# Kernel tuning notes

Hardware: AMD Instinct MI355X
Metric: run time of the kernel (lower is better)

The kernel has to match this reference:

```python
import jax, jax.numpy as jnp
import numpy as np

N, K, D = 32768, 32, 128


def setup_inputs() -> dict:
    key = jax.random.key(0)
    ks = jax.random.split(key, 8)
    return {
        "x1": jax.random.normal(ks[0], (N, D), dtype=jnp.float32),
        "dists_argmax_1": jax.random.randint(ks[1], (N, K), 0, N),
        "dists_max_1": jax.random.uniform(ks[2], (N, K), dtype=jnp.float32),
        "x2": jax.random.normal(ks[3], (N, D), dtype=jnp.float32),
        "dists_argmax_2": jax.random.randint(ks[4], (N, K), 0, N),
        "dists_max_2": jax.random.uniform(ks[5], (N, K), dtype=jnp.float32),
        "w_out": jax.random.normal(ks[6], (1, D), dtype=jnp.float32) * (1.0 / np.sqrt(D)),
        "b_out": jnp.zeros((1,), dtype=jnp.float32),
    }


def _branch(x, idx, dmax, w_out, b_out):
    # anchor gather: [N,K,D]
    anchor = x[idx]
    # mcf 'default': distance-scaled anchor features (self_features unused)
    msgs = dmax[..., None] * anchor  # [N,K,D]
    # linear_out_position then squeeze(-1): [N,K]
    out_pos = jnp.einsum("nkd,d->nk", msgs, w_out[0]) + b_out[0]
    # agg 'mean' over anchor dim: [N,D]
    out_struct = jnp.mean(msgs, axis=1)
    return out_pos, out_struct


def reference(x1, dists_argmax_1, dists_max_1, x2, dists_argmax_2, dists_max_2, w_out, b_out):
    op1, os1 = _branch(x1, dists_argmax_1, dists_max_1, w_out, b_out)
    op2, os2 = _branch(x2, dists_argmax_2, dists_max_2, w_out, b_out)
    return (op1, os1, op2, os2)
```

## Files before the change

### kernel.cpp

```cpp
#include <hip/hip_runtime.h>

#define NN 32768
#define KK 32
#define DD 128

typedef float v2f __attribute__((ext_vector_type(2)));
typedef float v4f __attribute__((ext_vector_type(4)));
typedef int   v4i __attribute__((ext_vector_type(4)));

__global__ __launch_bounds__(256) void prep_kernel(const float* __restrict__ x1,
                                                   const float* __restrict__ x2,
                                                   const float* __restrict__ w,
                                                   unsigned int* __restrict__ x8,
                                                   float* __restrict__ xw) {
    const int wave = threadIdx.x >> 6;
    const int lane = threadIdx.x & 63;
    const int half = lane >> 5;
    const int c    = lane & 31;
    const int row  = blockIdx.x * 8 + wave * 2 + half;
    const float* x = (row < NN) ? (x1 + (size_t)row * DD)
                                : (x2 + (size_t)(row - NN) * DD);
    const v4f xv = __builtin_nontemporal_load((const v4f*)(x + 4 * c));
    const float4 wv = *(const float4*)(w + 4 * c);

    int packed = __builtin_amdgcn_cvt_pk_fp8_f32(xv.x, xv.y, 0, false);
    packed     = __builtin_amdgcn_cvt_pk_fp8_f32(xv.z, xv.w, packed, true);
    x8[(size_t)row * 32 + c] = (unsigned int)packed;

    float s = xv.x * wv.x + xv.y * wv.y + xv.z * wv.z + xv.w * wv.w;
    #pragma unroll
    for (int m = 16; m >= 1; m >>= 1)
        s += __shfl_xor(s, m, 64);
    if (c == 0) xw[row] = s;
}

__global__ __launch_bounds__(256) void pgnn_main(
    const uint4* __restrict__ x8,
    const float* __restrict__ xw,
    const int* __restrict__ idx1, const float* __restrict__ dm1,
    const int* __restrict__ idx2, const float* __restrict__ dm2,
    const float* __restrict__ b_out,
    float* __restrict__ out)
{
    const int g      = blockIdx.x;
    const int xcd    = g & 7;
    const int branch = xcd >> 2;
    const int nb     = (g >> 3) * 4 + (xcd & 3);

    const uint4* __restrict__ xb  = x8 + (size_t)branch * NN * 8;
    const float* __restrict__ xwb = xw + (size_t)branch * NN;
    const int*   __restrict__ idx = branch ? idx2 : idx1;
    const float* __restrict__ dm  = branch ? dm2  : dm1;
    float* __restrict__ op = out + (size_t)branch * ((size_t)NN * KK + (size_t)NN * DD);
    float* __restrict__ os = op + (size_t)NN * KK;

    __shared__ uint2 s_pair[32][KK + 2];

    const int tid = threadIdx.x;
    const int n0  = nb * 32;

    {
        const int rr = tid >> 3;
        const int k4 = (tid & 7) * 4;
        const size_t off = (size_t)(n0 + rr) * KK + k4;
        const v4i iv = __builtin_nontemporal_load((const v4i*)(idx + off));
        const v4f dv = __builtin_nontemporal_load((const v4f*)(dm + off));
        const float bb = b_out[0];
        v4f o = { dv.x * xwb[iv.x] + bb, dv.y * xwb[iv.y] + bb,
                  dv.z * xwb[iv.z] + bb, dv.w * xwb[iv.w] + bb };
        __builtin_nontemporal_store(o, (v4f*)(op + off));
        s_pair[rr][k4 + 0] = make_uint2((unsigned)iv.x, __float_as_uint(dv.x));
        s_pair[rr][k4 + 1] = make_uint2((unsigned)iv.y, __float_as_uint(dv.y));
        s_pair[rr][k4 + 2] = make_uint2((unsigned)iv.z, __float_as_uint(dv.z));
        s_pair[rr][k4 + 3] = make_uint2((unsigned)iv.w, __float_as_uint(dv.w));
    }
    __syncthreads();

    const int sub = tid >> 3;
    const int h   = tid & 7;
    const uint2* __restrict__ prow = s_pair[sub];

    float a[16];
    #pragma unroll
    for (int i = 0; i < 16; ++i) a[i] = 0.f;

    #pragma unroll
    for (int kb = 0; kb < KK; kb += 4) {
        const uint4 pq0 = *(const uint4*)&prow[kb];
        const uint4 pq1 = *(const uint4*)&prow[kb + 2];
        uint4 u[4];
        u[0] = xb[pq0.x * 8u + h];
        u[1] = xb[pq0.z * 8u + h];
        u[2] = xb[pq1.x * 8u + h];
        u[3] = xb[pq1.z * 8u + h];
        const float dd4[4] = { __uint_as_float(pq0.y), __uint_as_float(pq0.w),
                               __uint_as_float(pq1.y), __uint_as_float(pq1.w) };
        #pragma unroll
        for (int j = 0; j < 4; ++j) {
            const float d = dd4[j];
            const v2f f0 = __builtin_amdgcn_cvt_pk_f32_fp8((int)u[j].x, false);
            const v2f f1 = __builtin_amdgcn_cvt_pk_f32_fp8((int)u[j].x, true);
            const v2f f2 = __builtin_amdgcn_cvt_pk_f32_fp8((int)u[j].y, false);
            const v2f f3 = __builtin_amdgcn_cvt_pk_f32_fp8((int)u[j].y, true);
            const v2f f4 = __builtin_amdgcn_cvt_pk_f32_fp8((int)u[j].z, false);
            const v2f f5 = __builtin_amdgcn_cvt_pk_f32_fp8((int)u[j].z, true);
            const v2f f6 = __builtin_amdgcn_cvt_pk_f32_fp8((int)u[j].w, false);
            const v2f f7 = __builtin_amdgcn_cvt_pk_f32_fp8((int)u[j].w, true);
            a[0]  += d * f0.x; a[1]  += d * f0.y; a[2]  += d * f1.x; a[3]  += d * f1.y;
            a[4]  += d * f2.x; a[5]  += d * f2.y; a[6]  += d * f3.x; a[7]  += d * f3.y;
            a[8]  += d * f4.x; a[9]  += d * f4.y; a[10] += d * f5.x; a[11] += d * f5.y;
            a[12] += d * f6.x; a[13] += d * f6.y; a[14] += d * f7.x; a[15] += d * f7.y;
        }
    }
    const float inv = 1.0f / KK;
    float* dst = os + (size_t)(n0 + sub) * DD + h * 16;
    v4f o0 = { a[0]  * inv, a[1]  * inv, a[2]  * inv, a[3]  * inv };
    v4f o1 = { a[4]  * inv, a[5]  * inv, a[6]  * inv, a[7]  * inv };
    v4f o2 = { a[8]  * inv, a[9]  * inv, a[10] * inv, a[11] * inv };
    v4f o3 = { a[12] * inv, a[13] * inv, a[14] * inv, a[15] * inv };
    __builtin_nontemporal_store(o0, (v4f*)dst);
    __builtin_nontemporal_store(o1, (v4f*)(dst + 4));
    __builtin_nontemporal_store(o2, (v4f*)(dst + 8));
    __builtin_nontemporal_store(o3, (v4f*)(dst + 12));
}

__global__ __launch_bounds__(256) void pgnn_fused(
    const float* __restrict__ x1, const int* __restrict__ idx1,
    const float* __restrict__ dm1,
    const float* __restrict__ x2, const int* __restrict__ idx2,
    const float* __restrict__ dm2,
    const float* __restrict__ w, const float* __restrict__ b_out,
    float* __restrict__ out)
{
    const int branch = blockIdx.y;
    const float* __restrict__ x   = branch ? x2   : x1;
    const int*   __restrict__ idx = branch ? idx2 : idx1;
    const float* __restrict__ dm  = branch ? dm2  : dm1;
    float* __restrict__ op = out + (size_t)branch * ((size_t)NN * KK + (size_t)NN * DD);
    float* __restrict__ os = op + (size_t)NN * KK;

    __shared__ int    s_idx[2][KK];
    __shared__ float  s_dm [2][KK];
    __shared__ float  s_dot[2][KK];
    __shared__ float4 s_acc[2][128];

    const int sub = threadIdx.x >> 7;
    const int t   = threadIdx.x & 127;
    const int gg  = t >> 5;
    const int c   = t & 31;
    const int n   = blockIdx.x * 2 + sub;

    if (t < KK) {
        s_idx[sub][t] = idx[(size_t)n * KK + t];
        s_dm [sub][t] = dm [(size_t)n * KK + t];
    }
    const float4 wv = *(const float4*)(w + 4 * c);
    __syncthreads();

    float4 acc = make_float4(0.f, 0.f, 0.f, 0.f);
    #pragma unroll
    for (int k0 = 0; k0 < KK / 4; ++k0) {
        const int   kk  = k0 * 4 + gg;
        const int   r   = s_idx[sub][kk];
        const float dmk = s_dm [sub][kk];
        const float4 v  = *(const float4*)(x + (size_t)r * DD + 4 * c);
        acc.x += dmk * v.x; acc.y += dmk * v.y;
        acc.z += dmk * v.z; acc.w += dmk * v.w;
        float p = v.x * wv.x + v.y * wv.y + v.z * wv.z + v.w * wv.w;
        #pragma unroll
        for (int m = 16; m >= 1; m >>= 1)
            p += __shfl_xor(p, m, 64);
        if (c == 0) s_dot[sub][kk] = p;
    }
    s_acc[sub][t] = acc;
    __syncthreads();

    if (t < KK)
        op[(size_t)n * KK + t] = s_dm[sub][t] * s_dot[sub][t] + b_out[0];
    if (t < 32) {
        const float4 b0 = s_acc[sub][t];
        const float4 b1 = s_acc[sub][32 + t];
        const float4 b2 = s_acc[sub][64 + t];
        const float4 b3 = s_acc[sub][96 + t];
        float4 r;
        r.x = (b0.x + b1.x + b2.x + b3.x) * (1.0f / KK);
        r.y = (b0.y + b1.y + b2.y + b3.y) * (1.0f / KK);
        r.z = (b0.z + b1.z + b2.z + b3.z) * (1.0f / KK);
        r.w = (b0.w + b1.w + b2.w + b3.w) * (1.0f / KK);
        *(float4*)(os + (size_t)n * DD + 4 * t) = r;
    }
}

extern "C" void kernel_launch(void* const* d_in, const int* in_sizes, int n_in,
                              void* d_out, int out_size, void* d_ws, size_t ws_size,
                              hipStream_t stream) {
    const float* x1   = (const float*)d_in[0];
    const int*   idx1 = (const int*)  d_in[1];
    const float* dm1  = (const float*)d_in[2];
    const float* x2   = (const float*)d_in[3];
    const int*   idx2 = (const int*)  d_in[4];
    const float* dm2  = (const float*)d_in[5];
    const float* w    = (const float*)d_in[6];
    const float* b    = (const float*)d_in[7];
    float* out = (float*)d_out;

    const size_t need = (size_t)2 * NN * DD
                      + (size_t)2 * NN * sizeof(float);
    if (ws_size >= need) {
        unsigned int* x8 = (unsigned int*)d_ws;
        float*        xw = (float*)((char*)d_ws + (size_t)2 * NN * DD);
        prep_kernel<<<dim3(2 * NN / 8), dim3(256), 0, stream>>>(x1, x2, w, x8, xw);
        pgnn_main<<<dim3(2 * NN / 32), dim3(256), 0, stream>>>(
            (const uint4*)x8, xw, idx1, dm1, idx2, dm2, b, out);
    } else {
        pgnn_fused<<<dim3(NN / 2, 2), dim3(256), 0, stream>>>(
            x1, idx1, dm1, x2, idx2, dm2, w, b, out);
    }
}
```

Baseline: 135.6 us.

## Split FP8 feature table by D-half so each XCD gathers from smaller slice

The fp8 copy of x is laid out as four planes (branch × half of D), each 64 bytes per row, and each XCD pair works on one branch/half combination. Each block now handles 64 rows for one D-half, so the gather working set per XCD shrinks to 2 MB, which is meant to fit better in the per-XCD L2 and raise the hit rate on random gathers. The trade-off is that idx and dmax are loaded twice (once per half), and out_pos is written only by the half-0 blocks.

```diff
diff --git a/kernel.cpp b/kernel.cpp
--- a/kernel.cpp
+++ b/kernel.cpp
@@ -15,17 +15,20 @@
                                                    float* __restrict__ xw) {
     const int wave = threadIdx.x >> 6;
     const int lane = threadIdx.x & 63;
-    const int half = lane >> 5;
+    const int rsel = lane >> 5;
     const int c    = lane & 31;
-    const int row  = blockIdx.x * 8 + wave * 2 + half;
-    const float* x = (row < NN) ? (x1 + (size_t)row * DD)
-                                : (x2 + (size_t)(row - NN) * DD);
+    const int row  = blockIdx.x * 8 + wave * 2 + rsel;
+    const int b    = (row >= NN);
+    const int r    = b ? row - NN : row;
+    const float* x = (b ? x2 : x1) + (size_t)r * DD;
     const v4f xv = __builtin_nontemporal_load((const v4f*)(x + 4 * c));
     const float4 wv = *(const float4*)(w + 4 * c);
 
     int packed = __builtin_amdgcn_cvt_pk_fp8_f32(xv.x, xv.y, 0, false);
     packed     = __builtin_amdgcn_cvt_pk_fp8_f32(xv.z, xv.w, packed, true);
-    x8[(size_t)row * 32 + c] = (unsigned int)packed;
+    const int dhalf = c >> 4;
+    const int cc    = c & 15;
+    x8[((size_t)(b * 2 + dhalf) * NN + r) * 16 + cc] = (unsigned int)packed;
 
     float s = xv.x * wv.x + xv.y * wv.y + xv.z * wv.z + xv.w * wv.w;
     #pragma unroll
@@ -44,40 +47,54 @@
 {
     const int g      = blockIdx.x;
     const int xcd    = g & 7;
-    const int branch = xcd >> 2;
-    const int nb     = (g >> 3) * 4 + (xcd & 3);
-
-    const uint4* __restrict__ xb  = x8 + (size_t)branch * NN * 8;
+    const int combo  = xcd >> 1;
+    const int branch = combo >> 1;
+    const int half   = combo & 1;
+    const int nb     = (g >> 3) * 2 + (xcd & 1);
+
+    const uint4* __restrict__ xbh = x8 + (size_t)combo * NN * 4;
     const float* __restrict__ xwb = xw + (size_t)branch * NN;
     const int*   __restrict__ idx = branch ? idx2 : idx1;
     const float* __restrict__ dm  = branch ? dm2  : dm1;
     float* __restrict__ op = out + (size_t)branch * ((size_t)NN * KK + (size_t)NN * DD);
     float* __restrict__ os = op + (size_t)NN * KK;
 
-    __shared__ uint2 s_pair[32][KK + 2];
+    __shared__ uint2 s_pair[64][KK + 2];
 
     const int tid = threadIdx.x;
-    const int n0  = nb * 32;
+    const int n0  = nb * 64;
 
     {
-        const int rr = tid >> 3;
-        const int k4 = (tid & 7) * 4;
-        const size_t off = (size_t)(n0 + rr) * KK + k4;
-        const v4i iv = __builtin_nontemporal_load((const v4i*)(idx + off));
-        const v4f dv = __builtin_nontemporal_load((const v4f*)(dm + off));
-        const float bb = b_out[0];
-        v4f o = { dv.x * xwb[iv.x] + bb, dv.y * xwb[iv.y] + bb,
-                  dv.z * xwb[iv.z] + bb, dv.w * xwb[iv.w] + bb };
-        __builtin_nontemporal_store(o, (v4f*)(op + off));
-        s_pair[rr][k4 + 0] = make_uint2((unsigned)iv.x, __float_as_uint(dv.x));
-        s_pair[rr][k4 + 1] = make_uint2((unsigned)iv.y, __float_as_uint(dv.y));
-        s_pair[rr][k4 + 2] = make_uint2((unsigned)iv.z, __float_as_uint(dv.z));
-        s_pair[rr][k4 + 3] = make_uint2((unsigned)iv.w, __float_as_uint(dv.w));
+        const int rr = tid >> 2;
+        const int k8 = (tid & 3) * 8;
+        const size_t off = (size_t)(n0 + rr) * KK + k8;
+        const v4i iv0 = __builtin_nontemporal_load((const v4i*)(idx + off));
+        const v4i iv1 = __builtin_nontemporal_load((const v4i*)(idx + off + 4));
+        const v4f dv0 = __builtin_nontemporal_load((const v4f*)(dm + off));
+        const v4f dv1 = __builtin_nontemporal_load((const v4f*)(dm + off + 4));
+        uint4* srow = (uint4*)&s_pair[rr][k8];
+        srow[0] = make_uint4((unsigned)iv0.x, __float_as_uint(dv0.x),
+                             (unsigned)iv0.y, __float_as_uint(dv0.y));
+        srow[1] = make_uint4((unsigned)iv0.z, __float_as_uint(dv0.z),
+                             (unsigned)iv0.w, __float_as_uint(dv0.w));
+        srow[2] = make_uint4((unsigned)iv1.x, __float_as_uint(dv1.x),
+                             (unsigned)iv1.y, __float_as_uint(dv1.y));
+        srow[3] = make_uint4((unsigned)iv1.z, __float_as_uint(dv1.z),
+                             (unsigned)iv1.w, __float_as_uint(dv1.w));
+        if (half == 0) {
+            const float bb = b_out[0];
+            v4f o0 = { dv0.x * xwb[iv0.x] + bb, dv0.y * xwb[iv0.y] + bb,
+                       dv0.z * xwb[iv0.z] + bb, dv0.w * xwb[iv0.w] + bb };
+            v4f o1 = { dv1.x * xwb[iv1.x] + bb, dv1.y * xwb[iv1.y] + bb,
+                       dv1.z * xwb[iv1.z] + bb, dv1.w * xwb[iv1.w] + bb };
+            __builtin_nontemporal_store(o0, (v4f*)(op + off));
+            __builtin_nontemporal_store(o1, (v4f*)(op + off + 4));
+        }
     }
     __syncthreads();
 
-    const int sub = tid >> 3;
-    const int h   = tid & 7;
+    const int sub = tid >> 2;
+    const int h   = tid & 3;
     const uint2* __restrict__ prow = s_pair[sub];
 
     float a[16];
@@ -89,10 +106,10 @@
         const uint4 pq0 = *(const uint4*)&prow[kb];
         const uint4 pq1 = *(const uint4*)&prow[kb + 2];
         uint4 u[4];
-        u[0] = xb[pq0.x * 8u + h];
-        u[1] = xb[pq0.z * 8u + h];
-        u[2] = xb[pq1.x * 8u + h];
-        u[3] = xb[pq1.z * 8u + h];
+        u[0] = xbh[pq0.x * 4u + h];
+        u[1] = xbh[pq0.z * 4u + h];
+        u[2] = xbh[pq1.x * 4u + h];
+        u[3] = xbh[pq1.z * 4u + h];
         const float dd4[4] = { __uint_as_float(pq0.y), __uint_as_float(pq0.w),
                                __uint_as_float(pq1.y), __uint_as_float(pq1.w) };
         #pragma unroll
@@ -113,7 +130,7 @@
         }
     }
     const float inv = 1.0f / KK;
-    float* dst = os + (size_t)(n0 + sub) * DD + h * 16;
+    float* dst = os + (size_t)(n0 + sub) * DD + half * 64 + h * 16;
     v4f o0 = { a[0]  * inv, a[1]  * inv, a[2]  * inv, a[3]  * inv };
     v4f o1 = { a[4]  * inv, a[5]  * inv, a[6]  * inv, a[7]  * inv };
     v4f o2 = { a[8]  * inv, a[9]  * inv, a[10] * inv, a[11] * inv };
```

After: 148.2 us. 1.09x slower.

## Split position-output pass into separate kernel and drop LDS staging in gather

Applied to the files above, without the earlier changes.

Moves the per-anchor position output (dmax times precomputed x·w plus bias) into its own streaming kernel, and has the gather kernel read idx/dmax directly from global memory instead of staging them through shared memory with a barrier. The gather kernel also gets a launch-bounds occupancy hint of 8 blocks. This removes the LDS round-trip and __syncthreads from the gather path and aims for higher occupancy. In exchange it adds a kernel launch and reads idx/dmax twice from memory, with eight threads per row issuing redundant loads.

```diff
diff --git a/kernel.cpp b/kernel.cpp
--- a/kernel.cpp
+++ b/kernel.cpp
@@ -34,51 +34,58 @@
     if (c == 0) xw[row] = s;
 }
 
-__global__ __launch_bounds__(256) void pgnn_main(
-    const uint4* __restrict__ x8,
+__global__ __launch_bounds__(256) void op_kernel(
     const float* __restrict__ xw,
     const int* __restrict__ idx1, const float* __restrict__ dm1,
     const int* __restrict__ idx2, const float* __restrict__ dm2,
     const float* __restrict__ b_out,
     float* __restrict__ out)
 {
+    const int bid    = blockIdx.x;
+    const int branch = bid >> 9;
+    const int lb     = bid & 511;
+    const float* __restrict__ xwb = xw + (size_t)branch * NN;
+    const int*   __restrict__ idx = branch ? idx2 : idx1;
+    const float* __restrict__ dm  = branch ? dm2  : dm1;
+    float* __restrict__ op = out + (size_t)branch * ((size_t)NN * KK + (size_t)NN * DD);
+
+    const size_t base = ((size_t)lb * 256 + threadIdx.x) * 8;
+    const v4i i0 = __builtin_nontemporal_load((const v4i*)(idx + base));
+    const v4i i1 = __builtin_nontemporal_load((const v4i*)(idx + base + 4));
+    const v4f d0 = __builtin_nontemporal_load((const v4f*)(dm + base));
+    const v4f d1 = __builtin_nontemporal_load((const v4f*)(dm + base + 4));
+    const float bb = b_out[0];
+    v4f o0 = { d0.x * xwb[i0.x] + bb, d0.y * xwb[i0.y] + bb,
+               d0.z * xwb[i0.z] + bb, d0.w * xwb[i0.w] + bb };
+    v4f o1 = { d1.x * xwb[i1.x] + bb, d1.y * xwb[i1.y] + bb,
+               d1.z * xwb[i1.z] + bb, d1.w * xwb[i1.w] + bb };
+    __builtin_nontemporal_store(o0, (v4f*)(op + base));
+    __builtin_nontemporal_store(o1, (v4f*)(op + base + 4));
+}
+
+__global__ __launch_bounds__(256, 8) void pgnn_gather(
+    const uint4* __restrict__ x8,
+    const int* __restrict__ idx1, const float* __restrict__ dm1,
+    const int* __restrict__ idx2, const float* __restrict__ dm2,
+    float* __restrict__ out)
+{
     const int g      = blockIdx.x;
     const int xcd    = g & 7;
     const int branch = xcd >> 2;
     const int nb     = (g >> 3) * 4 + (xcd & 3);
 
     const uint4* __restrict__ xb  = x8 + (size_t)branch * NN * 8;
-    const float* __restrict__ xwb = xw + (size_t)branch * NN;
     const int*   __restrict__ idx = branch ? idx2 : idx1;
     const float* __restrict__ dm  = branch ? dm2  : dm1;
-    float* __restrict__ op = out + (size_t)branch * ((size_t)NN * KK + (size_t)NN * DD);
-    float* __restrict__ os = op + (size_t)NN * KK;
-
-    __shared__ uint2 s_pair[32][KK + 2];
+    float* __restrict__ os = out + (size_t)branch * ((size_t)NN * KK + (size_t)NN * DD)
+                                 + (size_t)NN * KK;
 
     const int tid = threadIdx.x;
-    const int n0  = nb * 32;
-
-    {
-        const int rr = tid >> 3;
-        const int k4 = (tid & 7) * 4;
-        const size_t off = (size_t)(n0 + rr) * KK + k4;
-        const v4i iv = __builtin_nontemporal_load((const v4i*)(idx + off));
-        const v4f dv = __builtin_nontemporal_load((const v4f*)(dm + off));
-        const float bb = b_out[0];
-        v4f o = { dv.x * xwb[iv.x] + bb, dv.y * xwb[iv.y] + bb,
-                  dv.z * xwb[iv.z] + bb, dv.w * xwb[iv.w] + bb };
-        __builtin_nontemporal_store(o, (v4f*)(op + off));
-        s_pair[rr][k4 + 0] = make_uint2((unsigned)iv.x, __float_as_uint(dv.x));
-        s_pair[rr][k4 + 1] = make_uint2((unsigned)iv.y, __float_as_uint(dv.y));
-        s_pair[rr][k4 + 2] = make_uint2((unsigned)iv.z, __float_as_uint(dv.z));
-        s_pair[rr][k4 + 3] = make_uint2((unsigned)iv.w, __float_as_uint(dv.w));
-    }
-    __syncthreads();
-
     const int sub = tid >> 3;
     const int h   = tid & 7;
-    const uint2* __restrict__ prow = s_pair[sub];
+    const int row = nb * 32 + sub;
+    const int*   __restrict__ ip = idx + (size_t)row * KK;
+    const float* __restrict__ dp = dm  + (size_t)row * KK;
 
     float a[16];
     #pragma unroll
@@ -86,15 +93,14 @@
 
     #pragma unroll
     for (int kb = 0; kb < KK; kb += 4) {
-        const uint4 pq0 = *(const uint4*)&prow[kb];
-        const uint4 pq1 = *(const uint4*)&prow[kb + 2];
+        const v4i iv = *(const v4i*)(ip + kb);
+        const v4f dv = *(const v4f*)(dp + kb);
         uint4 u[4];
-        u[0] = xb[pq0.x * 8u + h];
-        u[1] = xb[pq0.z * 8u + h];
-        u[2] = xb[pq1.x * 8u + h];
-        u[3] = xb[pq1.z * 8u + h];
-        const float dd4[4] = { __uint_as_float(pq0.y), __uint_as_float(pq0.w),
-                               __uint_as_float(pq1.y), __uint_as_float(pq1.w) };
+        u[0] = xb[(unsigned)iv.x * 8u + h];
+        u[1] = xb[(unsigned)iv.y * 8u + h];
+        u[2] = xb[(unsigned)iv.z * 8u + h];
+        u[3] = xb[(unsigned)iv.w * 8u + h];
+        const float dd4[4] = { dv.x, dv.y, dv.z, dv.w };
         #pragma unroll
         for (int j = 0; j < 4; ++j) {
             const float d = dd4[j];
@@ -113,7 +119,7 @@
         }
     }
     const float inv = 1.0f / KK;
-    float* dst = os + (size_t)(n0 + sub) * DD + h * 16;
+    float* dst = os + (size_t)row * DD + h * 16;
     v4f o0 = { a[0]  * inv, a[1]  * inv, a[2]  * inv, a[3]  * inv };
     v4f o1 = { a[4]  * inv, a[5]  * inv, a[6]  * inv, a[7]  * inv };
     v4f o2 = { a[8]  * inv, a[9]  * inv, a[10] * inv, a[11] * inv };
@@ -210,8 +216,10 @@
         unsigned int* x8 = (unsigned int*)d_ws;
         float*        xw = (float*)((char*)d_ws + (size_t)2 * NN * DD);
         prep_kernel<<<dim3(2 * NN / 8), dim3(256), 0, stream>>>(x1, x2, w, x8, xw);
-        pgnn_main<<<dim3(2 * NN / 32), dim3(256), 0, stream>>>(
-            (const uint4*)x8, xw, idx1, dm1, idx2, dm2, b, out);
+        op_kernel<<<dim3(1024), dim3(256), 0, stream>>>(
+            xw, idx1, dm1, idx2, dm2, b, out);
+        pgnn_gather<<<dim3(2 * NN / 32), dim3(256), 0, stream>>>(
+            (const uint4*)x8, idx1, dm1, idx2, dm2, out);
     } else {
         pgnn_fused<<<dim3(NN / 2, 2), dim3(256), 0, stream>>>(
             x1, idx1, dm1, x2, idx2, dm2, w, b, out);
```

Measured after the change: 395.2 us. 2.91x slower.
